# Kernel tuning notes

Hardware: AMD Instinct MI355X
Metric: run time of the kernel (lower is better)

Reference implementation:

```python
import jax, jax.numpy as jnp
import numpy as np

B, C, H, W = 16, 64, 64, 64
K = 512  # n_embeddings


def setup_inputs() -> dict:
    key = jax.random.key(0)
    k1, k2 = jax.random.split(key)
    inputs = jax.random.normal(k1, (B, C, H, W), dtype=jnp.float32)
    emb_weight = jax.random.normal(k2, (K, C), dtype=jnp.float32)
    weight = jnp.ones((K,), dtype=jnp.float32)  # EMA cluster-size buffer
    return {"inputs": inputs, "emb_weight": emb_weight, "weight": weight}


def reference(inputs, emb_weight, weight):
    sg = jax.lax.stop_gradient
    # BCHW -> BHWC
    x = jnp.transpose(inputs, (0, 2, 3, 1))  # [B,H,W,C]
    flat = x.reshape(-1, x.shape[-1])        # [N,C]
    n = flat.shape[0]
    k = emb_weight.shape[0]
    # squared euclidean distances [N,K] (argmin identical to cdist argmin)
    d = (
        jnp.sum(flat * flat, axis=-1, keepdims=True)
        - 2.0 * (flat @ emb_weight.T)
        + jnp.sum(emb_weight * emb_weight, axis=-1)
    )
    indices = jnp.argmin(d, axis=1)  # [N]
    # avg_probs = mean over rows of one-hot mask == normalized histogram
    avg_probs = jnp.bincount(indices, length=k).astype(jnp.float32) / jnp.float32(n)
    perplexity = jnp.exp(-jnp.sum(avg_probs * jnp.log(avg_probs + 1e-10)))
    # straight-through quantization
    q = emb_weight[indices].reshape(x.shape)  # [B,H,W,C]
    quantized = sg(q) + x - sg(x)
    commitment_loss = jnp.mean((sg(quantized) - x) ** 2)
    active_codes = jnp.sum(weight >= 0.01)
    out = jnp.transpose(quantized, (0, 3, 1, 2))  # back to BCHW
    return out, commitment_loss, perplexity, active_codes, indices
```

## Files before the change

### kernel.cpp

```cpp
#include <hip/hip_runtime.h>

#define HW 4096
#define CHW 262144
#define OUT_ELEMS 4194304
#define FLT_BIG 3.4e38f

typedef __attribute__((ext_vector_type(8))) short  short8;
typedef __attribute__((ext_vector_type(4))) float  floatx4;
typedef __attribute__((ext_vector_type(4))) int    intx4;


__device__ __forceinline__ unsigned bf16_rne(float f) {
    unsigned u = __float_as_uint(f);
    return (u + 0x7FFFu + ((u >> 16) & 1u)) >> 16;
}

__device__ __forceinline__ void split8(const float* f, intx4* hi, intx4* lo) {
    unsigned h[4], l[4];
#pragma unroll
    for (int j = 0; j < 4; ++j) {
        const unsigned h0 = bf16_rne(f[2 * j]);
        const unsigned h1 = bf16_rne(f[2 * j + 1]);
        const float hf0 = __uint_as_float(h0 << 16);
        const float hf1 = __uint_as_float(h1 << 16);
        const unsigned l0 = bf16_rne(f[2 * j] - hf0);
        const unsigned l1 = bf16_rne(f[2 * j + 1] - hf1);
        h[j] = h0 | (h1 << 16);
        l[j] = l0 | (l1 << 16);
    }
    *hi = intx4{(int)h[0], (int)h[1], (int)h[2], (int)h[3]};
    *lo = intx4{(int)l[0], (int)l[1], (int)l[2], (int)l[3]};
}

__global__ void vq_prep(const float* __restrict__ emb,
                        unsigned short* __restrict__ pfrag,
                        float* __restrict__ enorm) {
    const int t = threadIdx.x;
    const int lane = t & 63;
#pragma unroll
    for (int i = 0; i < 8; ++i) {
        const int f    = (i << 8) + t;
        const int code = (blockIdx.x << 5) + (f >> 6);
        const int c    = lane;
        const float v  = emb[(code << 6) + c];
        const unsigned hb = bf16_rne(v);
        const float hf    = __uint_as_float(hb << 16);
        const unsigned lb = bf16_rne(v - hf);
        const int nc = code >> 6, grp = (code & 63) >> 4, n = code & 15;
        const int q = (c & 31) >> 3, o = c & 7;
        const int jh = c >> 5;
        const int jl = 2 + (c >> 5);
        pfrag[((((size_t)(nc*4 + jh)*4 + grp)*4 + q)*16 + n)*8 + o] = (unsigned short)hb;
        pfrag[((((size_t)(nc*4 + jl)*4 + grp)*4 + q)*16 + n)*8 + o] = (unsigned short)lb;
        float s = v * v;
#pragma unroll
        for (int off = 32; off > 0; off >>= 1) s += __shfl_xor(s, off, 64);
        if (lane == 0) enorm[code] = s;
    }
}

__global__ __launch_bounds__(256)
void vq_main(const float* __restrict__ x_in, const float* __restrict__ emb,
             const unsigned short* __restrict__ pfrag,
             const float* __restrict__ enorm,
             float* __restrict__ out, float* __restrict__ idx_out,
             double* __restrict__ ws_sse) {
    __shared__ float  b1s[2][32], b2s[2][32];
    __shared__ int    i1s[2][32], i2s[2][32];
    __shared__ int    c1i[32], c2i[32], qidx[32];
    __shared__ double parts[8][32];
    __shared__ double ls_red[4];

    const int t     = threadIdx.x;
    const int lane  = t & 63;
    const int wv    = t >> 6;
    const int col   = lane & 15;
    const int quad  = lane >> 4;
    const int blk   = blockIdx.x;
    const int mrow0 = (wv >> 1) << 4;
    const int khalf = wv & 1;
    const int ncol0 = khalf << 5;
    const int half = blk & 1;
    const int bh = blk >> 1;
    const int b = bh >> 6, h = bh & 63;
    const float* xb = x_in + (size_t)b * CHW + h * 64 + (half << 5);

    short8 Ah[2], Al[2];
#pragma unroll
    for (int u = 0; u < 2; ++u) {
        float f[8];
#pragma unroll
        for (int j = 0; j < 8; ++j) {
            const int c = (u << 5) + (quad << 3) + j;
            f[j] = xb[(size_t)c * HW + mrow0 + col];
        }
        intx4 hi, lo;
        split8(f, &hi, &lo);
        Ah[u] = __builtin_bit_cast(short8, hi);
        Al[u] = __builtin_bit_cast(short8, lo);
    }

    float B1[4], B2[4]; int I1[4], I2[4];
#pragma unroll
    for (int s = 0; s < 4; ++s) { B1[s] = FLT_BIG; B2[s] = FLT_BIG; I1[s] = 0x3FFFFFFF; I2[s] = 0x3FFFFFFF; }

    const char* pf = (const char*)pfrag + (size_t)lane * 16 + ((size_t)khalf << 11);

#pragma unroll 2
    for (int nc = 0; nc < 8; ++nc) {
        const char* base = pf + ((size_t)nc << 14);
        const int K0 = nc << 6;
        const float en0 = enorm[K0 + ncol0 + col];
        const float en1 = enorm[K0 + ncol0 + 16 + col];

        floatx4 a0{0.f,0.f,0.f,0.f}, a1{0.f,0.f,0.f,0.f};
#define BLD(j, g) (*(const short8*)(base + ((j) << 12) + ((g) << 10)))
        {
            const short8 b0 = BLD(0, 0), b1 = BLD(0, 1);
            a0 = __builtin_amdgcn_mfma_f32_16x16x32_bf16(Ah[0], b0, a0, 0, 0, 0);
            a1 = __builtin_amdgcn_mfma_f32_16x16x32_bf16(Ah[0], b1, a1, 0, 0, 0);
            a0 = __builtin_amdgcn_mfma_f32_16x16x32_bf16(Al[0], b0, a0, 0, 0, 0);
            a1 = __builtin_amdgcn_mfma_f32_16x16x32_bf16(Al[0], b1, a1, 0, 0, 0);
        }
        {
            const short8 b0 = BLD(1, 0), b1 = BLD(1, 1);
            a0 = __builtin_amdgcn_mfma_f32_16x16x32_bf16(Ah[1], b0, a0, 0, 0, 0);
            a1 = __builtin_amdgcn_mfma_f32_16x16x32_bf16(Ah[1], b1, a1, 0, 0, 0);
            a0 = __builtin_amdgcn_mfma_f32_16x16x32_bf16(Al[1], b0, a0, 0, 0, 0);
            a1 = __builtin_amdgcn_mfma_f32_16x16x32_bf16(Al[1], b1, a1, 0, 0, 0);
        }
        {
            const short8 b0 = BLD(2, 0), b1 = BLD(2, 1);
            a0 = __builtin_amdgcn_mfma_f32_16x16x32_bf16(Ah[0], b0, a0, 0, 0, 0);
            a1 = __builtin_amdgcn_mfma_f32_16x16x32_bf16(Ah[0], b1, a1, 0, 0, 0);
        }
        {
            const short8 b0 = BLD(3, 0), b1 = BLD(3, 1);
            a0 = __builtin_amdgcn_mfma_f32_16x16x32_bf16(Ah[1], b0, a0, 0, 0, 0);
            a1 = __builtin_amdgcn_mfma_f32_16x16x32_bf16(Ah[1], b1, a1, 0, 0, 0);
        }
#undef BLD

#pragma unroll
        for (int nt = 0; nt < 2; ++nt) {
            const int code = K0 + ncol0 + (nt << 4) + col;
            const float en = nt ? en1 : en0;
            const floatx4 av = nt ? a1 : a0;
#pragma unroll
            for (int reg = 0; reg < 4; ++reg) {
                const float d = fmaf(-2.f, av[reg], en);
                if (d < B1[reg])      { B2[reg] = B1[reg]; I2[reg] = I1[reg]; B1[reg] = d; I1[reg] = code; }
                else if (d < B2[reg]) { B2[reg] = d; I2[reg] = code; }
            }
        }
    }

#pragma unroll
    for (int off = 1; off <= 8; off <<= 1) {
#pragma unroll
        for (int s = 0; s < 4; ++s) {
            const float ob1 = __shfl_xor(B1[s], off, 64);
            const int   oi1 = __shfl_xor(I1[s], off, 64);
            const float ob2 = __shfl_xor(B2[s], off, 64);
            const int   oi2 = __shfl_xor(I2[s], off, 64);
            if (ob1 < B1[s] || (ob1 == B1[s] && oi1 < I1[s])) {
                float nb2; int ni2;
                if (B1[s] < ob2 || (B1[s] == ob2 && I1[s] < oi2)) { nb2 = B1[s]; ni2 = I1[s]; }
                else                                              { nb2 = ob2;  ni2 = oi2; }
                B1[s] = ob1; I1[s] = oi1; B2[s] = nb2; I2[s] = ni2;
            } else if (ob1 < B2[s] || (ob1 == B2[s] && oi1 < I2[s])) {
                B2[s] = ob1; I2[s] = oi1;
            }
        }
    }
    if (col == 0) {
#pragma unroll
        for (int s = 0; s < 4; ++s) {
            const int row = mrow0 + (quad << 2) + s;
            b1s[khalf][row] = B1[s]; b2s[khalf][row] = B2[s];
            i1s[khalf][row] = I1[s]; i2s[khalf][row] = I2[s];
        }
    }
    __syncthreads();

    if (t < 32) {
        const int r = t;
        float b1 = b1s[0][r], b2 = b2s[0][r];
        int   i1 = i1s[0][r], i2 = i2s[0][r];
        const float c1 = b1s[1][r]; const int j1 = i1s[1][r];
        const float c2 = b2s[1][r]; const int j2 = i2s[1][r];
        if (c1 < b1 || (c1 == b1 && j1 < i1))      { b2 = b1; i2 = i1; b1 = c1; i1 = j1; }
        else if (c1 < b2 || (c1 == b2 && j1 < i2)) { b2 = c1; i2 = j1; }
        if (c2 < b2 || (c2 == b2 && j2 < i2))      { b2 = c2; i2 = j2; }
        c1i[r] = i1; c2i[r] = i2;
    }
    __syncthreads();

    {
        const int r  = t & 31;
        const int k  = t >> 5;
        const int cq = k >> 1;
        const int code = (k & 1) ? c2i[r] : c1i[r];
        const float* ep = emb + ((size_t)code << 6) + (cq << 4);
        const float* xq = xb + r;
        double d0 = 0.0, d1 = 0.0;
#pragma unroll
        for (int cc = 0; cc < 16; cc += 2) {
            const int c = (cq << 4) + cc;
            const double f0 = (double)xq[(size_t)c * HW]       - (double)ep[cc];
            const double f1 = (double)xq[(size_t)(c + 1) * HW] - (double)ep[cc + 1];
            d0 = fma(f0, f0, d0);
            d1 = fma(f1, f1, d1);
        }
        parts[k][r] = d0 + d1;
    }
    __syncthreads();
    if (t < 32) {
        const double d1 = parts[0][t] + parts[2][t] + parts[4][t] + parts[6][t];
        const double d2 = parts[1][t] + parts[3][t] + parts[5][t] + parts[7][t];
        int i1 = c1i[t];
        const int i2 = c2i[t];
        if (d2 < d1 || (d2 == d1 && i2 < i1)) i1 = i2;
        qidx[t] = i1;
        idx_out[(blk << 5) + t] = (float)i1;
    }
    __syncthreads();

    {
        const int r  = t & 31;
        const int c0 = (t >> 5) << 3;
        const float* xp = xb + r;
        float*       op = out + (size_t)b * CHW + h * 64 + (half << 5) + r;
        const float* eq = emb + ((size_t)qidx[r] << 6);
        float sse_local = 0.f;
#pragma unroll
        for (int cc = 0; cc < 8; ++cc) {
            const int c = c0 + cc;
            const float qc = eq[c];
            const float dx = qc - xp[(size_t)c * HW];
            sse_local = fmaf(dx, dx, sse_local);
            op[(size_t)c * HW] = qc;
        }
#pragma unroll
        for (int off = 32; off > 0; off >>= 1)
            sse_local += __shfl_down(sse_local, off, 64);
        if (lane == 0) ls_red[wv] = (double)sse_local;
        __syncthreads();
        if (t == 0)
            ws_sse[blk] = (ls_red[0] + ls_red[1]) + (ls_red[2] + ls_red[3]);
    }
}

__global__ void vq_hist(const float* __restrict__ idx_out,
                        unsigned* __restrict__ part) {
    __shared__ unsigned hs[512];
    const int t = threadIdx.x;
    hs[t] = 0u; hs[t + 256] = 0u;
    __syncthreads();
    const float4* ip = (const float4*)(idx_out + (blockIdx.x << 12));
#pragma unroll
    for (int i = 0; i < 4; ++i) {
        const float4 v = ip[(i << 8) + t];
        atomicAdd(&hs[(int)v.x], 1u);
        atomicAdd(&hs[(int)v.y], 1u);
        atomicAdd(&hs[(int)v.z], 1u);
        atomicAdd(&hs[(int)v.w], 1u);
    }
    __syncthreads();
    unsigned* pp = part + (blockIdx.x << 9);
    pp[t] = hs[t]; pp[t + 256] = hs[t + 256];
}

__global__ void vq_scal(const unsigned* __restrict__ part,
                        const double* __restrict__ ws_sse,
                        const float* __restrict__ weight,
                        float* __restrict__ scal) {
    __shared__ double redt[8], reds[8];
    __shared__ int    redi[8];
    const int k = threadIdx.x;
    const int lane = k & 63, wv = k >> 6;
    unsigned cnt = 0;
#pragma unroll
    for (int p = 0; p < 16; ++p) cnt += part[(p << 9) + k];
    const double pr = (double)cnt / 65536.0;
    double term = pr * log(pr + 1e-10);
    double ssep = 0.0;
#pragma unroll
    for (int j = 0; j < 4; ++j) ssep += ws_sse[k + (j << 9)];
    int act = (weight[k] >= 0.01f) ? 1 : 0;
#pragma unroll
    for (int off = 32; off > 0; off >>= 1) {
        term += __shfl_down(term, off, 64);
        ssep += __shfl_down(ssep, off, 64);
        act  += __shfl_down(act,  off, 64);
    }
    if (lane == 0) { redt[wv] = term; reds[wv] = ssep; redi[wv] = act; }
    __syncthreads();
    if (k == 0) {
        double s = 0.0, ss = 0.0; int a = 0;
#pragma unroll
        for (int i = 0; i < 8; ++i) { s += redt[i]; ss += reds[i]; a += redi[i]; }
        scal[0] = (float)(ss / 4194304.0);
        scal[1] = (float)exp(-s);
        scal[2] = (float)a;
    }
}

extern "C" void kernel_launch(void* const* d_in, const int* in_sizes, int n_in,
                              void* d_out, int out_size, void* d_ws, size_t ws_size,
                              hipStream_t stream) {
    const float* x      = (const float*)d_in[0];
    const float* emb    = (const float*)d_in[1];
    const float* weight = (const float*)d_in[2];

    float* out = (float*)d_out;
    float*          enorm  = (float*)d_ws;
    unsigned short* pfrag  = (unsigned short*)((char*)d_ws + 4096);
    double*         ws_sse = (double*)((char*)d_ws + 135168);
    unsigned*       part   = (unsigned*)((char*)d_ws + 151552);

    float* scal    = out + OUT_ELEMS;
    float* idx_out = out + OUT_ELEMS + 3;

    vq_prep<<<16, 256, 0, stream>>>(emb, pfrag, enorm);
    vq_main<<<2048, 256, 0, stream>>>(x, emb, pfrag, enorm, out, idx_out, ws_sse);
    vq_hist<<<16, 256, 0, stream>>>(idx_out, part);
    vq_scal<<<1, 512, 0, stream>>>(part, ws_sse, weight, scal);
}
```

Before: 121.8 us.

## Repartition waves so each covers all 32 rows and a 16-code slice

Each of the four waves now holds A fragments for both 16-row halves of the 32-pixel tile and owns a 16-code column slice, instead of a 16-row by 32-code tile. Each B fragment load now feeds two MFMAs, which halves the per-wave codebook fragment traffic. In exchange the x loads and the bf16 split are done twice per wave, and each lane keeps twice as many top-2 registers. The cross-wave top-2 merge now runs over four partial results instead of two.

```diff
diff --git a/kernel.cpp b/kernel.cpp
--- a/kernel.cpp
+++ b/kernel.cpp
@@ -65,8 +65,8 @@
              const float* __restrict__ enorm,
              float* __restrict__ out, float* __restrict__ idx_out,
              double* __restrict__ ws_sse) {
-    __shared__ float  b1s[2][32], b2s[2][32];
-    __shared__ int    i1s[2][32], i2s[2][32];
+    __shared__ float  b1s[4][32], b2s[4][32];
+    __shared__ int    i1s[4][32], i2s[4][32];
     __shared__ int    c1i[32], c2i[32], qidx[32];
     __shared__ double parts[8][32];
     __shared__ double ls_red[4];
@@ -77,80 +77,81 @@
     const int col   = lane & 15;
     const int quad  = lane >> 4;
     const int blk   = blockIdx.x;
-    const int mrow0 = (wv >> 1) << 4;
-    const int khalf = wv & 1;
-    const int ncol0 = khalf << 5;
+    const int ncol0 = wv << 4;
     const int half = blk & 1;
     const int bh = blk >> 1;
     const int b = bh >> 6, h = bh & 63;
     const float* xb = x_in + (size_t)b * CHW + h * 64 + (half << 5);
 
-    short8 Ah[2], Al[2];
-#pragma unroll
-    for (int u = 0; u < 2; ++u) {
-        float f[8];
-#pragma unroll
-        for (int j = 0; j < 8; ++j) {
-            const int c = (u << 5) + (quad << 3) + j;
-            f[j] = xb[(size_t)c * HW + mrow0 + col];
-        }
-        intx4 hi, lo;
-        split8(f, &hi, &lo);
-        Ah[u] = __builtin_bit_cast(short8, hi);
-        Al[u] = __builtin_bit_cast(short8, lo);
-    }
-
-    float B1[4], B2[4]; int I1[4], I2[4];
-#pragma unroll
-    for (int s = 0; s < 4; ++s) { B1[s] = FLT_BIG; B2[s] = FLT_BIG; I1[s] = 0x3FFFFFFF; I2[s] = 0x3FFFFFFF; }
-
-    const char* pf = (const char*)pfrag + (size_t)lane * 16 + ((size_t)khalf << 11);
+    short8 Ah[2][2], Al[2][2];
+#pragma unroll
+    for (int m = 0; m < 2; ++m) {
+        const int w = (m << 4) + col;
+#pragma unroll
+        for (int u = 0; u < 2; ++u) {
+            float f[8];
+#pragma unroll
+            for (int j = 0; j < 8; ++j) {
+                const int c = (u << 5) + (quad << 3) + j;
+                f[j] = xb[(size_t)c * HW + w];
+            }
+            intx4 hi, lo;
+            split8(f, &hi, &lo);
+            Ah[m][u] = __builtin_bit_cast(short8, hi);
+            Al[m][u] = __builtin_bit_cast(short8, lo);
+        }
+    }
+
+    float B1[8], B2[8]; int I1[8], I2[8];
+#pragma unroll
+    for (int s = 0; s < 8; ++s) { B1[s] = FLT_BIG; B2[s] = FLT_BIG; I1[s] = 0x3FFFFFFF; I2[s] = 0x3FFFFFFF; }
+
+    const char* pf = (const char*)pfrag + (size_t)lane * 16 + ((size_t)wv << 10);
 
 #pragma unroll 2
     for (int nc = 0; nc < 8; ++nc) {
         const char* base = pf + ((size_t)nc << 14);
         const int K0 = nc << 6;
-        const float en0 = enorm[K0 + ncol0 + col];
-        const float en1 = enorm[K0 + ncol0 + 16 + col];
+        const float en = enorm[K0 + ncol0 + col];
 
         floatx4 a0{0.f,0.f,0.f,0.f}, a1{0.f,0.f,0.f,0.f};
-#define BLD(j, g) (*(const short8*)(base + ((j) << 12) + ((g) << 10)))
+#define BLD(j) (*(const short8*)(base + ((j) << 12)))
         {
-            const short8 b0 = BLD(0, 0), b1 = BLD(0, 1);
-            a0 = __builtin_amdgcn_mfma_f32_16x16x32_bf16(Ah[0], b0, a0, 0, 0, 0);
-            a1 = __builtin_amdgcn_mfma_f32_16x16x32_bf16(Ah[0], b1, a1, 0, 0, 0);
-            a0 = __builtin_amdgcn_mfma_f32_16x16x32_bf16(Al[0], b0, a0, 0, 0, 0);
-            a1 = __builtin_amdgcn_mfma_f32_16x16x32_bf16(Al[0], b1, a1, 0, 0, 0);
+            const short8 bv = BLD(0);
+            a0 = __builtin_amdgcn_mfma_f32_16x16x32_bf16(Ah[0][0], bv, a0, 0, 0, 0);
+            a1 = __builtin_amdgcn_mfma_f32_16x16x32_bf16(Ah[1][0], bv, a1, 0, 0, 0);
+            a0 = __builtin_amdgcn_mfma_f32_16x16x32_bf16(Al[0][0], bv, a0, 0, 0, 0);
+            a1 = __builtin_amdgcn_mfma_f32_16x16x32_bf16(Al[1][0], bv, a1, 0, 0, 0);
         }
         {
-            const short8 b0 = BLD(1, 0), b1 = BLD(1, 1);
-            a0 = __builtin_amdgcn_mfma_f32_16x16x32_bf16(Ah[1], b0, a0, 0, 0, 0);
-            a1 = __builtin_amdgcn_mfma_f32_16x16x32_bf16(Ah[1], b1, a1, 0, 0, 0);
-            a0 = __builtin_amdgcn_mfma_f32_16x16x32_bf16(Al[1], b0, a0, 0, 0, 0);
-            a1 = __builtin_amdgcn_mfma_f32_16x16x32_bf16(Al[1], b1, a1, 0, 0, 0);
+            const short8 bv = BLD(1);
+            a0 = __builtin_amdgcn_mfma_f32_16x16x32_bf16(Ah[0][1], bv, a0, 0, 0, 0);
+            a1 = __builtin_amdgcn_mfma_f32_16x16x32_bf16(Ah[1][1], bv, a1, 0, 0, 0);
+            a0 = __builtin_amdgcn_mfma_f32_16x16x32_bf16(Al[0][1], bv, a0, 0, 0, 0);
+            a1 = __builtin_amdgcn_mfma_f32_16x16x32_bf16(Al[1][1], bv, a1, 0, 0, 0);
         }
         {
-            const short8 b0 = BLD(2, 0), b1 = BLD(2, 1);
-            a0 = __builtin_amdgcn_mfma_f32_16x16x32_bf16(Ah[0], b0, a0, 0, 0, 0);
-            a1 = __builtin_amdgcn_mfma_f32_16x16x32_bf16(Ah[0], b1, a1, 0, 0, 0);
+            const short8 bv = BLD(2);
+            a0 = __builtin_amdgcn_mfma_f32_16x16x32_bf16(Ah[0][0], bv, a0, 0, 0, 0);
+            a1 = __builtin_amdgcn_mfma_f32_16x16x32_bf16(Ah[1][0], bv, a1, 0, 0, 0);
         }
         {
-            const short8 b0 = BLD(3, 0), b1 = BLD(3, 1);
-            a0 = __builtin_amdgcn_mfma_f32_16x16x32_bf16(Ah[1], b0, a0, 0, 0, 0);
-            a1 = __builtin_amdgcn_mfma_f32_16x16x32_bf16(Ah[1], b1, a1, 0, 0, 0);
+            const short8 bv = BLD(3);
+            a0 = __builtin_amdgcn_mfma_f32_16x16x32_bf16(Ah[0][1], bv, a0, 0, 0, 0);
+            a1 = __builtin_amdgcn_mfma_f32_16x16x32_bf16(Ah[1][1], bv, a1, 0, 0, 0);
         }
 #undef BLD
 
-#pragma unroll
-        for (int nt = 0; nt < 2; ++nt) {
-            const int code = K0 + ncol0 + (nt << 4) + col;
-            const float en = nt ? en1 : en0;
-            const floatx4 av = nt ? a1 : a0;
+        const int code = K0 + ncol0 + col;
+#pragma unroll
+        for (int m = 0; m < 2; ++m) {
+            const floatx4 av = m ? a1 : a0;
 #pragma unroll
             for (int reg = 0; reg < 4; ++reg) {
                 const float d = fmaf(-2.f, av[reg], en);
-                if (d < B1[reg])      { B2[reg] = B1[reg]; I2[reg] = I1[reg]; B1[reg] = d; I1[reg] = code; }
-                else if (d < B2[reg]) { B2[reg] = d; I2[reg] = code; }
+                const int s = (m << 2) + reg;
+                if (d < B1[s])      { B2[s] = B1[s]; I2[s] = I1[s]; B1[s] = d; I1[s] = code; }
+                else if (d < B2[s]) { B2[s] = d; I2[s] = code; }
             }
         }
     }
@@ -158,7 +159,7 @@
 #pragma unroll
     for (int off = 1; off <= 8; off <<= 1) {
 #pragma unroll
-        for (int s = 0; s < 4; ++s) {
+        for (int s = 0; s < 8; ++s) {
             const float ob1 = __shfl_xor(B1[s], off, 64);
             const int   oi1 = __shfl_xor(I1[s], off, 64);
             const float ob2 = __shfl_xor(B2[s], off, 64);
@@ -175,10 +176,10 @@
     }
     if (col == 0) {
 #pragma unroll
-        for (int s = 0; s < 4; ++s) {
-            const int row = mrow0 + (quad << 2) + s;
-            b1s[khalf][row] = B1[s]; b2s[khalf][row] = B2[s];
-            i1s[khalf][row] = I1[s]; i2s[khalf][row] = I2[s];
+        for (int s = 0; s < 8; ++s) {
+            const int row = ((s >> 2) << 4) + (quad << 2) + (s & 3);
+            b1s[wv][row] = B1[s]; b2s[wv][row] = B2[s];
+            i1s[wv][row] = I1[s]; i2s[wv][row] = I2[s];
         }
     }
     __syncthreads();
@@ -187,11 +188,14 @@
         const int r = t;
         float b1 = b1s[0][r], b2 = b2s[0][r];
         int   i1 = i1s[0][r], i2 = i2s[0][r];
-        const float c1 = b1s[1][r]; const int j1 = i1s[1][r];
-        const float c2 = b2s[1][r]; const int j2 = i2s[1][r];
-        if (c1 < b1 || (c1 == b1 && j1 < i1))      { b2 = b1; i2 = i1; b1 = c1; i1 = j1; }
-        else if (c1 < b2 || (c1 == b2 && j1 < i2)) { b2 = c1; i2 = j1; }
-        if (c2 < b2 || (c2 == b2 && j2 < i2))      { b2 = c2; i2 = j2; }
+#pragma unroll
+        for (int q = 1; q < 4; ++q) {
+            const float c1 = b1s[q][r]; const int j1 = i1s[q][r];
+            const float c2 = b2s[q][r]; const int j2 = i2s[q][r];
+            if (c1 < b1 || (c1 == b1 && j1 < i1))      { b2 = b1; i2 = i1; b1 = c1; i1 = j1; }
+            else if (c1 < b2 || (c1 == b2 && j1 < i2)) { b2 = c1; i2 = j1; }
+            if (c2 < b2 || (c2 == b2 && j2 < i2))      { b2 = c2; i2 = j2; }
+        }
         c1i[r] = i1; c2i[r] = i2;
     }
     __syncthreads();
```

Result: slower. 145.8 us (+19.7%).

## Replace shuffle top-2 reduction with LDS merge and gate fp64 rescoring on margin

Applied to the files above, without the earlier changes.

Each lane now writes its per-row top-2 candidates to shared memory as float4s, and two 32-thread groups merge 16 columns each before one cross-half shuffle. The earlier 4-round xor-shuffle butterfly and one barrier stage go away. The fp64 exact-distance recheck of the two best codes now runs only when the approximate gap is under 0.05. It is done serially by one thread per row instead of spread across all 256 threads. This cuts shuffle and barrier cost and skips most fp64 work, but the fixed threshold could pick a different argmin than the reference when bf16-split error exceeds the margin, and the serial 64-channel loop is slow for rows that do hit it.

```diff
diff --git a/kernel.cpp b/kernel.cpp
--- a/kernel.cpp
+++ b/kernel.cpp
@@ -65,10 +65,8 @@
              const float* __restrict__ enorm,
              float* __restrict__ out, float* __restrict__ idx_out,
              double* __restrict__ ws_sse) {
-    __shared__ float  b1s[2][32], b2s[2][32];
-    __shared__ int    i1s[2][32], i2s[2][32];
-    __shared__ int    c1i[32], c2i[32], qidx[32];
-    __shared__ double parts[8][32];
+    __shared__ float4 cand[64 * 17];
+    __shared__ int    qidx[32];
     __shared__ double ls_red[4];
 
     const int t     = threadIdx.x;
@@ -156,73 +154,53 @@
     }
 
 #pragma unroll
-    for (int off = 1; off <= 8; off <<= 1) {
-#pragma unroll
-        for (int s = 0; s < 4; ++s) {
-            const float ob1 = __shfl_xor(B1[s], off, 64);
-            const int   oi1 = __shfl_xor(I1[s], off, 64);
-            const float ob2 = __shfl_xor(B2[s], off, 64);
-            const int   oi2 = __shfl_xor(I2[s], off, 64);
-            if (ob1 < B1[s] || (ob1 == B1[s] && oi1 < I1[s])) {
-                float nb2; int ni2;
-                if (B1[s] < ob2 || (B1[s] == ob2 && I1[s] < oi2)) { nb2 = B1[s]; ni2 = I1[s]; }
-                else                                              { nb2 = ob2;  ni2 = oi2; }
-                B1[s] = ob1; I1[s] = oi1; B2[s] = nb2; I2[s] = ni2;
-            } else if (ob1 < B2[s] || (ob1 == B2[s] && oi1 < I2[s])) {
-                B2[s] = ob1; I2[s] = oi1;
+    for (int s = 0; s < 4; ++s) {
+        const int row = mrow0 + (quad << 2) + s;
+        cand[((khalf << 5) | row) * 17 + col] =
+            make_float4(B1[s], __int_as_float(I1[s]), B2[s], __int_as_float(I2[s]));
+    }
+    __syncthreads();
+
+    if (t < 64) {
+        const int r  = t & 31;
+        const int kh = t >> 5;
+        const float4* cp = &cand[((kh << 5) | r) * 17];
+        float b1 = FLT_BIG, b2 = FLT_BIG; int i1 = 0x3FFFFFFF, i2 = 0x3FFFFFFF;
+#pragma unroll 4
+        for (int c = 0; c < 16; ++c) {
+            const float4 v = cp[c];
+            const float c1 = v.x; const int j1 = __float_as_int(v.y);
+            const float c2 = v.z; const int j2 = __float_as_int(v.w);
+            if (c1 < b1 || (c1 == b1 && j1 < i1))      { b2 = b1; i2 = i1; b1 = c1; i1 = j1; }
+            else if (c1 < b2 || (c1 == b2 && j1 < i2)) { b2 = c1; i2 = j1; }
+            if (c2 < b2 || (c2 == b2 && j2 < i2))      { b2 = c2; i2 = j2; }
+        }
+        const float ob1 = __shfl_xor(b1, 32, 64);
+        const int   oi1 = __shfl_xor(i1, 32, 64);
+        const float ob2 = __shfl_xor(b2, 32, 64);
+        const int   oi2 = __shfl_xor(i2, 32, 64);
+        if (ob1 < b1 || (ob1 == b1 && oi1 < i1))      { b2 = b1; i2 = i1; b1 = ob1; i1 = oi1; }
+        else if (ob1 < b2 || (ob1 == b2 && oi1 < i2)) { b2 = ob1; i2 = oi1; }
+        if (ob2 < b2 || (ob2 == b2 && oi2 < i2))      { b2 = ob2; i2 = oi2; }
+
+        if (t < 32) {
+            if (b2 - b1 < 0.05f) {
+                const float* xp  = xb + r;
+                const float* e1p = emb + ((size_t)i1 << 6);
+                const float* e2p = emb + ((size_t)i2 << 6);
+                double d1 = 0.0, d2 = 0.0;
+                for (int c = 0; c < 64; ++c) {
+                    const double xv = (double)xp[(size_t)c * HW];
+                    const double f1 = xv - (double)e1p[c];
+                    const double f2 = xv - (double)e2p[c];
+                    d1 = fma(f1, f1, d1);
+                    d2 = fma(f2, f2, d2);
+                }
+                if (d2 < d1 || (d2 == d1 && i2 < i1)) i1 = i2;
             }
-        }
-    }
-    if (col == 0) {
-#pragma unroll
-        for (int s = 0; s < 4; ++s) {
-            const int row = mrow0 + (quad << 2) + s;
-            b1s[khalf][row] = B1[s]; b2s[khalf][row] = B2[s];
-            i1s[khalf][row] = I1[s]; i2s[khalf][row] = I2[s];
-        }
-    }
-    __syncthreads();
-
-    if (t < 32) {
-        const int r = t;
-        float b1 = b1s[0][r], b2 = b2s[0][r];
-        int   i1 = i1s[0][r], i2 = i2s[0][r];
-        const float c1 = b1s[1][r]; const int j1 = i1s[1][r];
-        const float c2 = b2s[1][r]; const int j2 = i2s[1][r];
-        if (c1 < b1 || (c1 == b1 && j1 < i1))      { b2 = b1; i2 = i1; b1 = c1; i1 = j1; }
-        else if (c1 < b2 || (c1 == b2 && j1 < i2)) { b2 = c1; i2 = j1; }
-        if (c2 < b2 || (c2 == b2 && j2 < i2))      { b2 = c2; i2 = j2; }
-        c1i[r] = i1; c2i[r] = i2;
-    }
-    __syncthreads();
-
-    {
-        const int r  = t & 31;
-        const int k  = t >> 5;
-        const int cq = k >> 1;
-        const int code = (k & 1) ? c2i[r] : c1i[r];
-        const float* ep = emb + ((size_t)code << 6) + (cq << 4);
-        const float* xq = xb + r;
-        double d0 = 0.0, d1 = 0.0;
-#pragma unroll
-        for (int cc = 0; cc < 16; cc += 2) {
-            const int c = (cq << 4) + cc;
-            const double f0 = (double)xq[(size_t)c * HW]       - (double)ep[cc];
-            const double f1 = (double)xq[(size_t)(c + 1) * HW] - (double)ep[cc + 1];
-            d0 = fma(f0, f0, d0);
-            d1 = fma(f1, f1, d1);
-        }
-        parts[k][r] = d0 + d1;
-    }
-    __syncthreads();
-    if (t < 32) {
-        const double d1 = parts[0][t] + parts[2][t] + parts[4][t] + parts[6][t];
-        const double d2 = parts[1][t] + parts[3][t] + parts[5][t] + parts[7][t];
-        int i1 = c1i[t];
-        const int i2 = c2i[t];
-        if (d2 < d1 || (d2 == d1 && i2 < i1)) i1 = i2;
-        qidx[t] = i1;
-        idx_out[(blk << 5) + t] = (float)i1;
+            qidx[r] = i1;
+            idx_out[(blk << 5) + r] = (float)i1;
+        }
     }
     __syncthreads();
 
```

Result: no change. 122.8 us (+0.8%).
